# Kernel tuning notes

Hardware: AMD Instinct MI355X
Metric: run time of the kernel (lower is better)

Reference implementation:

```python
import jax, jax.numpy as jnp
import numpy as np

IN_F = 4096
OUT_F = 4096
B, S = 4, 2048


def _quantize_weight(w_float):
    """Replicates Int4PackedLinear.__init__ double quantization; returns reg_b and w_scale."""
    w_amax = jnp.abs(w_float).max()
    scale = jnp.where(w_amax == 0, 1.0, w_amax / 127.0)
    w_int8 = jnp.clip(jnp.round(w_float / scale), -127, 127).astype(jnp.int8)
    low4_amax = jnp.abs(w_int8.astype(jnp.float32)).max()
    low4_scale = jnp.where(low4_amax == 0, 1.0, low4_amax / 7.0)
    w_low = jnp.clip(jnp.round(w_int8.astype(jnp.float32) / low4_scale), -7, 7).astype(jnp.int8)
    w_rec = jnp.round(w_low.astype(jnp.float32) * low4_scale).astype(jnp.int8)
    w_high = jnp.clip(w_int8.astype(jnp.int32) - w_rec.astype(jnp.int32), -7, 7).astype(jnp.int8)
    reg_b = (w_rec.astype(jnp.int32) + w_high.astype(jnp.int32)).astype(jnp.int8)  # w_combined
    return reg_b, scale.astype(jnp.float32)


def setup_inputs() -> dict:
    key = jax.random.key(0)
    k1, k2, k3 = jax.random.split(key, 3)
    w_float = jax.random.normal(k1, (OUT_F, IN_F), dtype=jnp.float32) * 0.02
    reg_b, w_scale = _quantize_weight(w_float)
    x = jax.random.normal(k2, (B, S, IN_F), dtype=jnp.float32)
    bias = jax.random.normal(k3, (OUT_F,), dtype=jnp.float32) * 0.01
    # gate=1.0 >= threshold=0.3 -> full-precision INT8 path uses reg_b
    return {"x": x, "w_int": reg_b, "w_scale": w_scale, "bias": bias}


def reference(x, w_int, w_scale, bias):
    # --- dynamic per-tensor activation quantization ---
    x_amax = jnp.abs(x).max()
    x_scale = jnp.where(x_amax == 0, jnp.float32(1.0), x_amax / 127.0)
    x_int8 = jnp.clip(jnp.round(x / x_scale), -127, 127).astype(jnp.int8)
    # --- integer matmul (accumulate in int32, like torch._int_mm) ---
    out_i32 = jnp.einsum(
        'bsk,nk->bsn',
        x_int8.astype(jnp.int32),
        w_int.astype(jnp.int32),
    )  # [B, S, OUT_F]
    # --- dequant scale in bf16 AFTER the integer matmul, then bias add ---
    combined_scale = (x_scale * w_scale).astype(jnp.bfloat16)
    out = out_i32.astype(jnp.bfloat16) * combined_scale
    out = out + bias  # bf16 + fp32 -> fp32, matching torch promotion
    return out
```

## Files before the change

### kernel.cpp

```cpp
#include <hip/hip_runtime.h>
#include <hip/hip_bf16.h>
#include <stdint.h>

#define IN_F  4096
#define OUT_F 4096
#define BSZ   4
#define SEQ   2048
#define MDIM  (BSZ * SEQ)

typedef __attribute__((address_space(1))) uint8_t ga_u8_t;
typedef __attribute__((address_space(3))) uint8_t ls_u8_t;

__device__ __forceinline__ void gload16_lds(const void* g, void* l) {
    __builtin_amdgcn_global_load_lds((ga_u8_t*)g, (ls_u8_t*)l, 16, 0, 0);
}

__device__ __forceinline__ float bf16_rne(float f) {
    unsigned u = __float_as_uint(f);
    u = (u + 0x7fffu + ((u >> 16) & 1u)) & 0xffff0000u;
    return __uint_as_float(u);
}

__global__ void amax_kernel(const float* __restrict__ x, int n4,
                            unsigned int* __restrict__ amax_u) {
    const float4* x4 = (const float4*)x;
    int idx = blockIdx.x * blockDim.x + threadIdx.x;
    int stride = gridDim.x * blockDim.x;
    float m = 0.0f;
    for (int i = idx; i < n4; i += stride) {
        float4 v = x4[i];
        m = fmaxf(m, fmaxf(fmaxf(fabsf(v.x), fabsf(v.y)),
                           fmaxf(fabsf(v.z), fabsf(v.w))));
    }
    for (int off = 32; off > 0; off >>= 1)
        m = fmaxf(m, __shfl_down(m, off, 64));
    __shared__ float sm[4];
    int lane = threadIdx.x & 63, wave = threadIdx.x >> 6;
    if (lane == 0) sm[wave] = m;
    __syncthreads();
    if (threadIdx.x == 0) {
        m = fmaxf(fmaxf(sm[0], sm[1]), fmaxf(sm[2], sm[3]));
        atomicMax(amax_u, __float_as_uint(m));
    }
}

__global__ void prep_kernel(const float* __restrict__ x,
                            const int* __restrict__ w,
                            signed char* __restrict__ x8,
                            signed char* __restrict__ w8,
                            const unsigned int* __restrict__ amax_u,
                            int nx4, int nw4) {
    int idx = blockIdx.x * blockDim.x + threadIdx.x;
    if (idx < nx4) {
        float amax = __uint_as_float(*amax_u);
        float xs = (amax == 0.0f) ? 1.0f : (amax / 127.0f);
        float4 v = ((const float4*)x)[idx];
        char4 q;
        q.x = (signed char)fminf(fmaxf(rintf(v.x / xs), -127.0f), 127.0f);
        q.y = (signed char)fminf(fmaxf(rintf(v.y / xs), -127.0f), 127.0f);
        q.z = (signed char)fminf(fmaxf(rintf(v.z / xs), -127.0f), 127.0f);
        q.w = (signed char)fminf(fmaxf(rintf(v.w / xs), -127.0f), 127.0f);
        ((char4*)x8)[idx] = q;
    } else {
        int widx = idx - nx4;
        if (widx < nw4) {
            int4 v = ((const int4*)w)[widx];
            char4 q;
            q.x = (signed char)v.x; q.y = (signed char)v.y;
            q.z = (signed char)v.z; q.w = (signed char)v.w;
            ((char4*)w8)[widx] = q;
        }
    }
}

using i32x4 = __attribute__((ext_vector_type(4))) int;

#define FENCE() asm volatile("" ::: "memory")
#define BAR()   do { FENCE(); __builtin_amdgcn_s_barrier(); FENCE(); } while (0)
#define WAITV(N) asm volatile("s_waitcnt vmcnt(" #N ")" ::: "memory")

#define TILE1(BUF, SBUF, KST, DOSTAGE, WV)                                   \
  {                                                                          \
    const signed char* base = smem + (BUF) * 32768;                          \
    BAR();                                                                   \
    if (DOSTAGE) {                                                           \
        signed char* sb = smem + (SBUF) * 32768;                             \
        gload16_lds(gA0 + (KST), sb + dA0);                                  \
        gload16_lds(gA1 + (KST), sb + dA1);                                  \
        gload16_lds(gB0 + (KST), sb + dB0);                                  \
        gload16_lds(gB1 + (KST), sb + dB1);                                  \
    }                                                                        \
    WV;                                                                      \
    i32x4 bF[4], aF[8];                                                      \
    _Pragma("unroll")                                                        \
    for (int j = 0; j < 4; ++j) bF[j] = *(const i32x4*)(base + boff[j]);     \
    _Pragma("unroll")                                                        \
    for (int i = 0; i < 8; ++i) aF[i] = *(const i32x4*)(base + aoff[i]);     \
    _Pragma("unroll")                                                        \
    for (int i = 0; i < 8; ++i)                                              \
      _Pragma("unroll")                                                      \
      for (int j = 0; j < 4; ++j)                                            \
        acc[i][j] = __builtin_amdgcn_mfma_i32_16x16x64_i8(                   \
            aF[i], bF[j], acc[i][j], 0, 0, 0);                               \
  }

__global__ __launch_bounds__(512, 2) void gemm_i8_kernel(
    const signed char* __restrict__ A,
    const signed char* __restrict__ B,
    const unsigned int* __restrict__ amax_u,
    const float* __restrict__ wscale_p,
    const float* __restrict__ bias,
    float* __restrict__ out) {
    __shared__ signed char smem[3 * 32768];

    const int tid = threadIdx.x;
    const int lane = tid & 63;
    const int wave = tid >> 6;
    const int wm = wave >> 2;
    const int wn = wave & 3;

    const int bid = blockIdx.x;
    const int wg = (bid & 7) * 64 + (bid >> 3);
    const int mt = wg >> 4;
    const int nt = wg & 15;
    const int tileM = mt * 256;
    const int tileN = nt * 256;

    const int g = tid;
    const int srow = g >> 2;
    const int scol = ((g & 3) ^ ((srow >> 1) & 3)) * 16;
    const signed char* gA0 = A + (size_t)(tileM +       srow) * IN_F + scol;
    const signed char* gA1 = A + (size_t)(tileM + 128 + srow) * IN_F + scol;
    const signed char* gB0 = B + (size_t)(tileN +       srow) * IN_F + scol;
    const signed char* gB1 = B + (size_t)(tileN + 128 + srow) * IN_F + scol;
    const int dA0 = g * 16;
    const int dA1 = 8192  + g * 16;
    const int dB0 = 16384 + g * 16;
    const int dB1 = 24576 + g * 16;

    int aoff[8], boff[4];
    const int kc = lane >> 4;
#pragma unroll
    for (int i = 0; i < 8; ++i) {
        int r = wm * 128 + i * 16 + (lane & 15);
        aoff[i] = r * 64 + ((kc ^ ((r >> 1) & 3)) * 16);
    }
#pragma unroll
    for (int j = 0; j < 4; ++j) {
        int r = wn * 64 + j * 16 + (lane & 15);
        boff[j] = 16384 + r * 64 + ((kc ^ ((r >> 1) & 3)) * 16);
    }

    i32x4 acc[8][4] = {};

    gload16_lds(gA0,      smem + dA0);
    gload16_lds(gA1,      smem + dA1);
    gload16_lds(gB0,      smem + dB0);
    gload16_lds(gB1,      smem + dB1);
    gload16_lds(gA0 + 64, smem + 32768 + dA0);
    gload16_lds(gA1 + 64, smem + 32768 + dA1);
    gload16_lds(gB0 + 64, smem + 32768 + dB0);
    gload16_lds(gB1 + 64, smem + 32768 + dB1);
    WAITV(4);

    for (int kt = 0; kt < 60; kt += 3) {
        TILE1(0, 2, (kt + 2) * 64, 1, WAITV(4));
        TILE1(1, 0, (kt + 3) * 64, 1, WAITV(4));
        TILE1(2, 1, (kt + 4) * 64, 1, WAITV(4));
    }
    TILE1(0, 2, 62 * 64, 1, WAITV(4));
    TILE1(1, 0, 63 * 64, 1, WAITV(4));
    TILE1(2, 0, 0,       0, WAITV(0));
    TILE1(0, 0, 0,       0, (void)0);

    float amax = __uint_as_float(*amax_u);
    float xs = (amax == 0.0f) ? 1.0f : (amax / 127.0f);
    float cs = bf16_rne(xs * wscale_p[0]);

#pragma unroll
    for (int j = 0; j < 4; ++j) {
        int n = tileN + wn * 64 + j * 16 + (lane & 15);
        float bz = bias[n];
#pragma unroll
        for (int i = 0; i < 8; ++i) {
            int row0 = tileM + wm * 128 + i * 16 + (lane >> 4) * 4;
#pragma unroll
            for (int r = 0; r < 4; ++r) {
                float v = bf16_rne((float)acc[i][j][r]);
                float p = bf16_rne(v * cs);
                __builtin_nontemporal_store(
                    p + bz, &out[(size_t)(row0 + r) * OUT_F + n]);
            }
        }
    }
}

extern "C" void kernel_launch(void* const* d_in, const int* in_sizes, int n_in,
                              void* d_out, int out_size, void* d_ws,
                              size_t ws_size, hipStream_t stream) {
    const float* x = (const float*)d_in[0];
    const int* w_int = (const int*)d_in[1];
    const float* w_scale = (const float*)d_in[2];
    const float* bias = (const float*)d_in[3];
    float* out = (float*)d_out;

    unsigned char* ws = (unsigned char*)d_ws;
    unsigned int* amax_u = (unsigned int*)ws;
    signed char* w8 = (signed char*)(ws + 64);
    signed char* x8 = (signed char*)(ws + 64 + (size_t)OUT_F * IN_F);

    hipMemsetAsync(amax_u, 0, 4, stream);

    const int n_x4 = MDIM * IN_F / 4;
    const int n_w4 = OUT_F * IN_F / 4;

    amax_kernel<<<4096, 256, 0, stream>>>(x, n_x4, amax_u);
    prep_kernel<<<(n_x4 + n_w4) / 256, 256, 0, stream>>>(
        x, w_int, x8, w8, amax_u, n_x4, n_w4);

    const int nblocks = (MDIM / 256) * (OUT_F / 256);
    gemm_i8_kernel<<<nblocks, 512, 0, stream>>>(x8, w8, amax_u, w_scale, bias,
                                                out);
}
```

Baseline: 433.2 us.

## Pre-pack weights into MFMA fragment layout and load B directly to registers

```diff
diff --git a/kernel.cpp b/kernel.cpp
--- a/kernel.cpp
+++ b/kernel.cpp
@@ -47,9 +47,9 @@
 __global__ void prep_kernel(const float* __restrict__ x,
                             const int* __restrict__ w,
                             signed char* __restrict__ x8,
-                            signed char* __restrict__ w8,
+                            signed char* __restrict__ w8p,
                             const unsigned int* __restrict__ amax_u,
-                            int nx4, int nw4) {
+                            int nx4, int nwt) {
     int idx = blockIdx.x * blockDim.x + threadIdx.x;
     if (idx < nx4) {
         float amax = __uint_as_float(*amax_u);
@@ -63,12 +63,24 @@
         ((char4*)x8)[idx] = q;
     } else {
         int widx = idx - nx4;
-        if (widx < nw4) {
-            int4 v = ((const int4*)w)[widx];
-            char4 q;
-            q.x = (signed char)v.x; q.y = (signed char)v.y;
-            q.z = (signed char)v.z; q.w = (signed char)v.w;
-            ((char4*)w8)[widx] = q;
+        if (widx < nwt) {
+            int lane = widx & 63;
+            int kt   = (widx >> 6) & 63;
+            int n16  = widx >> 12;
+            int r  = n16 * 16 + (lane & 15);
+            int kb = kt * 64 + (lane >> 4) * 16;
+            const int4* src = (const int4*)(w + (size_t)r * IN_F + kb);
+            int4 v0 = src[0], v1 = src[1], v2 = src[2], v3 = src[3];
+            int p0 = (v0.x & 255) | ((v0.y & 255) << 8) |
+                     ((v0.z & 255) << 16) | ((int)((unsigned)(v0.w & 255) << 24));
+            int p1 = (v1.x & 255) | ((v1.y & 255) << 8) |
+                     ((v1.z & 255) << 16) | ((int)((unsigned)(v1.w & 255) << 24));
+            int p2 = (v2.x & 255) | ((v2.y & 255) << 8) |
+                     ((v2.z & 255) << 16) | ((int)((unsigned)(v2.w & 255) << 24));
+            int p3 = (v3.x & 255) | ((v3.y & 255) << 8) |
+                     ((v3.z & 255) << 16) | ((int)((unsigned)(v3.w & 255) << 24));
+            int4 out; out.x = p0; out.y = p1; out.z = p2; out.w = p3;
+            ((int4*)w8p)[widx] = out;
         }
     }
 }
@@ -79,21 +91,22 @@
 #define BAR()   do { FENCE(); __builtin_amdgcn_s_barrier(); FENCE(); } while (0)
 #define WAITV(N) asm volatile("s_waitcnt vmcnt(" #N ")" ::: "memory")
 
-#define TILE1(BUF, SBUF, KST, DOSTAGE, WV)                                   \
+#define TILEX(BUF, SBUF, KST, KTN, BC, BN, DOSTAGE, DOPREF)                  \
   {                                                                          \
-    const signed char* base = smem + (BUF) * 32768;                          \
     BAR();                                                                   \
     if (DOSTAGE) {                                                           \
-        signed char* sb = smem + (SBUF) * 32768;                             \
+        signed char* sb = smem + (SBUF) * 16384;                             \
         gload16_lds(gA0 + (KST), sb + dA0);                                  \
         gload16_lds(gA1 + (KST), sb + dA1);                                  \
-        gload16_lds(gB0 + (KST), sb + dB0);                                  \
-        gload16_lds(gB1 + (KST), sb + dB1);                                  \
     }                                                                        \
-    WV;                                                                      \
-    i32x4 bF[4], aF[8];                                                      \
-    _Pragma("unroll")                                                        \
-    for (int j = 0; j < 4; ++j) bF[j] = *(const i32x4*)(base + boff[j]);     \
+    FENCE();      \
+    if (DOPREF) {                                                            \
+        _Pragma("unroll")                                                    \
+        for (int j = 0; j < 4; ++j)                                          \
+            BN[j] = *(const i32x4*)(wbase + j * 65536 + (KTN) * 1024);       \
+    }                                                                        \
+    const signed char* base = smem + (BUF) * 16384;                          \
+    i32x4 aF[8];                                                             \
     _Pragma("unroll")                                                        \
     for (int i = 0; i < 8; ++i) aF[i] = *(const i32x4*)(base + aoff[i]);     \
     _Pragma("unroll")                                                        \
@@ -101,7 +114,7 @@
       _Pragma("unroll")                                                      \
       for (int j = 0; j < 4; ++j)                                            \
         acc[i][j] = __builtin_amdgcn_mfma_i32_16x16x64_i8(                   \
-            aF[i], bF[j], acc[i][j], 0, 0, 0);                               \
+            aF[i], BC[j], acc[i][j], 0, 0, 0);                               \
   }
 
 __global__ __launch_bounds__(512, 2) void gemm_i8_kernel(
@@ -111,7 +124,7 @@
     const float* __restrict__ wscale_p,
     const float* __restrict__ bias,
     float* __restrict__ out) {
-    __shared__ signed char smem[3 * 32768];
+    __shared__ signed char smem[3 * 16384];
 
     const int tid = threadIdx.x;
     const int lane = tid & 63;
@@ -131,47 +144,45 @@
     const int scol = ((g & 3) ^ ((srow >> 1) & 3)) * 16;
     const signed char* gA0 = A + (size_t)(tileM +       srow) * IN_F + scol;
     const signed char* gA1 = A + (size_t)(tileM + 128 + srow) * IN_F + scol;
-    const signed char* gB0 = B + (size_t)(tileN +       srow) * IN_F + scol;
-    const signed char* gB1 = B + (size_t)(tileN + 128 + srow) * IN_F + scol;
     const int dA0 = g * 16;
-    const int dA1 = 8192  + g * 16;
-    const int dB0 = 16384 + g * 16;
-    const int dB1 = 24576 + g * 16;
-
-    int aoff[8], boff[4];
+    const int dA1 = 8192 + g * 16;
+
+    int aoff[8];
     const int kc = lane >> 4;
 #pragma unroll
     for (int i = 0; i < 8; ++i) {
         int r = wm * 128 + i * 16 + (lane & 15);
         aoff[i] = r * 64 + ((kc ^ ((r >> 1) & 3)) * 16);
     }
-#pragma unroll
-    for (int j = 0; j < 4; ++j) {
-        int r = wn * 64 + j * 16 + (lane & 15);
-        boff[j] = 16384 + r * 64 + ((kc ^ ((r >> 1) & 3)) * 16);
-    }
+
+    const signed char* wbase =
+        B + (size_t)(nt * 16 + wn * 4) * 65536 + lane * 16;
 
     i32x4 acc[8][4] = {};
+    i32x4 b0[4], b1[4];
 
     gload16_lds(gA0,      smem + dA0);
     gload16_lds(gA1,      smem + dA1);
-    gload16_lds(gB0,      smem + dB0);
-    gload16_lds(gB1,      smem + dB1);
-    gload16_lds(gA0 + 64, smem + 32768 + dA0);
-    gload16_lds(gA1 + 64, smem + 32768 + dA1);
-    gload16_lds(gB0 + 64, smem + 32768 + dB0);
-    gload16_lds(gB1 + 64, smem + 32768 + dB1);
-    WAITV(4);
-
-    for (int kt = 0; kt < 60; kt += 3) {
-        TILE1(0, 2, (kt + 2) * 64, 1, WAITV(4));
-        TILE1(1, 0, (kt + 3) * 64, 1, WAITV(4));
-        TILE1(2, 1, (kt + 4) * 64, 1, WAITV(4));
-    }
-    TILE1(0, 2, 62 * 64, 1, WAITV(4));
-    TILE1(1, 0, 63 * 64, 1, WAITV(4));
-    TILE1(2, 0, 0,       0, WAITV(0));
-    TILE1(0, 0, 0,       0, (void)0);
+    gload16_lds(gA0 + 64, smem + 16384 + dA0);
+    gload16_lds(gA1 + 64, smem + 16384 + dA1);
+    FENCE();
+#pragma unroll
+    for (int j = 0; j < 4; ++j)
+        b0[j] = *(const i32x4*)(wbase + j * 65536);
+    WAITV(6);
+
+    for (int kt = 0; kt < 60; kt += 6) {
+        TILEX(0, 2, (kt + 2) * 64, kt + 1, b0, b1, 1, 1);
+        TILEX(1, 0, (kt + 3) * 64, kt + 2, b1, b0, 1, 1);
+        TILEX(2, 1, (kt + 4) * 64, kt + 3, b0, b1, 1, 1);
+        TILEX(0, 2, (kt + 5) * 64, kt + 4, b1, b0, 1, 1);
+        TILEX(1, 0, (kt + 6) * 64, kt + 5, b0, b1, 1, 1);
+        TILEX(2, 1, (kt + 7) * 64, kt + 6, b1, b0, 1, 1);
+    }
+    TILEX(0, 2, 62 * 64, 61, b0, b1, 1, 1);
+    TILEX(1, 0, 63 * 64, 62, b1, b0, 1, 1);
+    TILEX(2, 0, 0,       63, b0, b1, 0, 1);
+    TILEX(0, 0, 0,       0,  b1, b0, 0, 0);
 
     float amax = __uint_as_float(*amax_u);
     float xs = (amax == 0.0f) ? 1.0f : (amax / 127.0f);
@@ -206,19 +217,19 @@
 
     unsigned char* ws = (unsigned char*)d_ws;
     unsigned int* amax_u = (unsigned int*)ws;
-    signed char* w8 = (signed char*)(ws + 64);
+    signed char* w8p = (signed char*)(ws + 64);
     signed char* x8 = (signed char*)(ws + 64 + (size_t)OUT_F * IN_F);
 
     hipMemsetAsync(amax_u, 0, 4, stream);
 
     const int n_x4 = MDIM * IN_F / 4;
-    const int n_w4 = OUT_F * IN_F / 4;
+    const int n_wt = 256 * 64 * 64;
 
     amax_kernel<<<4096, 256, 0, stream>>>(x, n_x4, amax_u);
-    prep_kernel<<<(n_x4 + n_w4) / 256, 256, 0, stream>>>(
-        x, w_int, x8, w8, amax_u, n_x4, n_w4);
+    prep_kernel<<<(n_x4 + n_wt + 255) / 256, 256, 0, stream>>>(
+        x, w_int, x8, w8p, amax_u, n_x4, n_wt);
 
     const int nblocks = (MDIM / 256) * (OUT_F / 256);
-    gemm_i8_kernel<<<nblocks, 512, 0, stream>>>(x8, w8, amax_u, w_scale, bias,
+    gemm_i8_kernel<<<nblocks, 512, 0, stream>>>(x8, w8p, amax_u, w_scale, bias,
                                                 out);
 }
```

Measured after the change: 445.2 us. +2.8%, slower.
